# Performance work log

Hardware: AMD Instinct MI355X
Metric: run time of the kernel (lower is better)

Reference implementation:

```python
import jax, jax.numpy as jnp
import numpy as np
import math

Z_DIM = 128
N_HEAD = 4
C = 32
L = 512


def setup_inputs() -> dict:
    key = jax.random.key(0)
    ks = jax.random.split(key, 16)
    s = lambda fan_in: 1.0 / math.sqrt(fan_in)
    hc = N_HEAD * C
    return {
        "z_": jax.random.normal(ks[0], (L, L, Z_DIM), dtype=jnp.float32),
        "ln_g": jnp.ones((Z_DIM,), jnp.float32),
        "ln_b": jnp.zeros((Z_DIM,), jnp.float32),
        "qw": jax.random.normal(ks[1], (Z_DIM, hc), jnp.float32) * s(Z_DIM),
        "qb": jnp.zeros((hc,), jnp.float32),
        "kw": jax.random.normal(ks[2], (Z_DIM, hc), jnp.float32) * s(Z_DIM),
        "kb": jnp.zeros((hc,), jnp.float32),
        "vw": jax.random.normal(ks[3], (Z_DIM, hc), jnp.float32) * s(Z_DIM),
        "vb": jnp.zeros((hc,), jnp.float32),
        "bw": jax.random.normal(ks[4], (Z_DIM, N_HEAD), jnp.float32) * s(Z_DIM),
        "bb": jnp.zeros((N_HEAD,), jnp.float32),
        "gw": jax.random.normal(ks[5], (Z_DIM, hc), jnp.float32) * s(Z_DIM),
        "gb": jnp.zeros((hc,), jnp.float32),
        "ow": jax.random.normal(ks[6], (hc, Z_DIM), jnp.float32) * s(hc),
        "ob": jnp.zeros((Z_DIM,), jnp.float32),
    }


def _layernorm(x, g, b, eps=1e-5):
    mu = jnp.mean(x, axis=-1, keepdims=True)
    var = jnp.var(x, axis=-1, keepdims=True)
    return (x - mu) * jax.lax.rsqrt(var + eps) * g + b


def reference(z_, ln_g, ln_b, qw, qb, kw, kb, vw, vb, bw, bb, gw, gb, ow, ob):
    L1, L2, D = z_.shape
    z = _layernorm(z_, ln_g, ln_b)
    q = (z @ qw + qb).reshape(L1, L2, N_HEAD, C)
    k = (z @ kw + kb).reshape(L1, L2, N_HEAD, C)
    v = (z @ vw + vb).reshape(L1, L2, N_HEAD, C)
    bias = z @ bw + bb  # [L1, L2, H]
    scale = (1.0 / math.sqrt(C)) / math.sqrt(L2)
    # Note: reduction over the leading (row) axis b, per the source einsum.
    att = jnp.einsum('blhc,bkhc->lkh', q, k) * scale + bias  # [L, L, H]
    att = jax.nn.softmax(att, axis=1)
    o = jnp.einsum('lkh,bkhc->blhc', att, v)  # [L1, L2, H, C]
    g = jax.nn.sigmoid((z @ gw + gb).reshape(L1, L2, N_HEAD, C))
    o = (g * o).reshape(L1, L2, N_HEAD * C)
    return o @ ow + ob
```

## Files before the change

### kernel.cpp

```cpp
#include <hip/hip_runtime.h>
#include <hip/hip_bf16.h>
#include <math.h>


#define LL 512
#define ZD 128
#define NROWS (LL*LL)
#define ATT_SCALE (1.0f/128.0f)
#define NSPLIT 8

typedef __attribute__((ext_vector_type(4))) float f32x4;
typedef __attribute__((ext_vector_type(8))) short short8;
typedef __attribute__((ext_vector_type(8))) unsigned short u16x8;

__device__ __forceinline__ unsigned short f2bf(float f){
  union { float f; unsigned u; } v; v.f = f;
  unsigned r = (v.u + 0x7FFFu + ((v.u >> 16) & 1u)) >> 16;
  return (unsigned short)r;
}
__device__ __forceinline__ float bf2f(unsigned short h){
  union { float f; unsigned u; } v; v.u = ((unsigned)h) << 16;
  return v.f;
}

__global__ void k_prep(const float* __restrict__ qw, const float* __restrict__ kw,
                       const float* __restrict__ vw, const float* __restrict__ gw,
                       const float* __restrict__ bw,
                       const float* __restrict__ qb, const float* __restrict__ kb,
                       const float* __restrict__ vb, const float* __restrict__ gb,
                       const float* __restrict__ bb,
                       const float* __restrict__ ow,
                       unsigned short* __restrict__ Wt, unsigned short* __restrict__ Ot,
                       float* __restrict__ biasv){
  int n = blockIdx.x;
  int k = threadIdx.x;
  if (n < 516){
    float v;
    if (n < 128)      v = qw[k*128 + n];
    else if (n < 256) v = kw[k*128 + (n-128)];
    else if (n < 384) v = vw[k*128 + (n-256)];
    else if (n < 512) v = gw[k*128 + (n-384)];
    else              v = bw[k*4   + (n-512)];
    Wt[n*ZD + k] = f2bf(v);
    if (k == 0){
      float bvv;
      if (n < 128)      bvv = qb[n];
      else if (n < 256) bvv = kb[n-128];
      else if (n < 384) bvv = vb[n-256];
      else if (n < 512) bvv = gb[n-384];
      else              bvv = bb[n-512];
      biasv[n] = bvv;
    }
  } else {
    int d = n - 516;
    Ot[d*ZD + k] = f2bf(ow[k*ZD + d]);
  }
}

__launch_bounds__(256, 3)
__global__ void k_proj(const float* __restrict__ z,
                       const float* __restrict__ ln_g, const float* __restrict__ ln_b,
                       const unsigned short* __restrict__ Wt,
                       const float* __restrict__ biasv,
                       unsigned short* __restrict__ qbuf,
                       unsigned short* __restrict__ kbuf,
                       unsigned short* __restrict__ vt,
                       unsigned short* __restrict__ gbuf,
                       float* __restrict__ biasz){
  const int P = 136;
  __shared__ unsigned short As[128*136];
  __shared__ float lng[128], lnb[128];
  __shared__ float lbias[640];
  int t = threadIdx.x;
  long mbase = (long)blockIdx.x * 128;
  int bb_ = (int)(mbase >> 9);
  int rr0 = (int)(mbase & 511);
  if (t < 128){ lng[t] = ln_g[t]; lnb[t] = ln_b[t]; }
  if (t < 160) *(float4*)&lbias[t*4] = *(const float4*)&biasv[t*4];
  {
    int row = t >> 1, half = t & 1;
    const float4* zr = (const float4*)(z + (mbase + row)*ZD + half*64);
    float4 zv[16];
    float s1 = 0.f, s2 = 0.f;
#pragma unroll
    for (int i = 0; i < 16; i++){
      zv[i] = zr[i];
      s1 += zv[i].x + zv[i].y + zv[i].z + zv[i].w;
      s2 += zv[i].x*zv[i].x + zv[i].y*zv[i].y + zv[i].z*zv[i].z + zv[i].w*zv[i].w;
    }
    s1 += __shfl_xor(s1, 1);
    s2 += __shfl_xor(s2, 1);
    float mu = s1 * (1.f/128.f);
    float rs = rsqrtf(s2*(1.f/128.f) - mu*mu + 1e-5f);
    __syncthreads();
#pragma unroll
    for (int i = 0; i < 16; i++){
      int c0 = half*64 + i*4;
      ushort4 pk;
      pk.x = f2bf((zv[i].x - mu)*rs*lng[c0+0] + lnb[c0+0]);
      pk.y = f2bf((zv[i].y - mu)*rs*lng[c0+1] + lnb[c0+1]);
      pk.z = f2bf((zv[i].z - mu)*rs*lng[c0+2] + lnb[c0+2]);
      pk.w = f2bf((zv[i].w - mu)*rs*lng[c0+3] + lnb[c0+3]);
      *(ushort4*)&As[row*P + c0] = pk;
    }
  }
  __syncthreads();
  int w = t >> 6, tl = t & 63;
  int m0 = (w & 1)*64, n0 = (w >> 1)*64;
  int lr = tl & 15, quad = tl >> 4;
#pragma unroll
  for (int nt = 0; nt < 5; nt++){
    f32x4 acc[4][4];
    for (int i=0;i<4;i++) for (int j=0;j<4;j++) acc[i][j] = f32x4{0.f,0.f,0.f,0.f};
    for (int kk = 0; kk < 4; kk++){
      short8 a[4], bq[4];
      for (int i=0;i<4;i++) a[i] = *(const short8*)&As[(m0 + i*16 + lr)*P + kk*32 + quad*8];
      const unsigned short* wp = Wt + ((long)nt*128 + n0 + lr)*ZD + kk*32 + quad*8;
      for (int j=0;j<4;j++) bq[j] = *(const short8*)(wp + (long)j*16*ZD);
      for (int i=0;i<4;i++) for (int j=0;j<4;j++){
        if (nt == 2) acc[i][j] = __builtin_amdgcn_mfma_f32_16x16x32_bf16(a[i], bq[j], acc[i][j], 0,0,0);
        else         acc[i][j] = __builtin_amdgcn_mfma_f32_16x16x32_bf16(bq[j], a[i], acc[i][j], 0,0,0);
      }
    }
    if (nt == 0 || nt == 1 || nt == 3){
      unsigned short* dst = (nt == 0) ? qbuf : (nt == 1) ? kbuf : gbuf;
      float4 bd[4];
#pragma unroll
      for (int j=0;j<4;j++) bd[j] = *(const float4*)&lbias[nt*128 + n0 + j*16 + quad*4];
#pragma unroll
      for (int i=0;i<4;i++){
        long grow = mbase + m0 + i*16 + lr;
#pragma unroll
        for (int j=0;j<4;j++){
          int nc0 = n0 + j*16 + quad*4;
          ushort4 pk;
          pk.x = f2bf(acc[i][j][0] + bd[j].x);
          pk.y = f2bf(acc[i][j][1] + bd[j].y);
          pk.z = f2bf(acc[i][j][2] + bd[j].z);
          pk.w = f2bf(acc[i][j][3] + bd[j].w);
          *(ushort4*)&dst[grow*128 + nc0] = pk;
        }
      }
    } else if (nt == 2){
#pragma unroll
      for (int j=0;j<4;j++){
        int ncol = n0 + j*16 + lr;
        float bv = lbias[256 + ncol];
#pragma unroll
        for (int i=0;i<4;i++){
          int rr = rr0 + m0 + i*16 + quad*4;
          ushort4 pk;
          pk.x = f2bf(acc[i][j][0] + bv);
          pk.y = f2bf(acc[i][j][1] + bv);
          pk.z = f2bf(acc[i][j][2] + bv);
          pk.w = f2bf(acc[i][j][3] + bv);
          *(ushort4*)&vt[((long)bb_*128 + ncol)*512 + rr] = pk;
        }
      }
    } else if (n0 == 0 && quad == 0){
      float4 bd = *(const float4*)&lbias[512];
#pragma unroll
      for (int i=0;i<4;i++){
        long grow = mbase + m0 + i*16 + lr;
        float4 o;
        o.x = acc[i][0][0] + bd.x;
        o.y = acc[i][0][1] + bd.y;
        o.z = acc[i][0][2] + bd.z;
        o.w = acc[i][0][3] + bd.w;
        *(float4*)&biasz[grow*4] = o;
      }
    }
  }
}

__launch_bounds__(256, 3)
__global__ void k_att(const unsigned short* __restrict__ qbuf,
                      const unsigned short* __restrict__ kbuf,
                      float* __restrict__ partial){
  int t = threadIdx.x;
  int ktb = blockIdx.x * 128, ltb = blockIdx.y * 128;
  int split = blockIdx.z >> 2, h = blockIdx.z & 3;
  int w = t >> 6, tl = t & 63;
  int m0 = (w & 1)*64, n0 = (w >> 1)*64;
  int lr = tl & 15, quad = tl >> 4;
  f32x4 acc[4][4];
  for (int i=0;i<4;i++) for (int j=0;j<4;j++) acc[i][j] = f32x4{0.f,0.f,0.f,0.f};
  for (int it = 0; it < 64; it++){
    int b = split*64 + it;
    long qb0 = ((long)b*LL + ltb + m0 + lr)*128 + h*32 + quad*8;
    long kb0 = ((long)b*LL + ktb + n0 + lr)*128 + h*32 + quad*8;
    short8 a[4], bq[4];
#pragma unroll
    for (int i=0;i<4;i++) a[i]  = *(const short8*)&qbuf[qb0 + (long)i*16*128];
#pragma unroll
    for (int i=0;i<4;i++) bq[i] = *(const short8*)&kbuf[kb0 + (long)i*16*128];
#pragma unroll
    for (int i=0;i<4;i++) for (int j=0;j<4;j++)
      acc[i][j] = __builtin_amdgcn_mfma_f32_16x16x32_bf16(a[i], bq[j], acc[i][j], 0,0,0);
  }
  long obase = (((long)(split*4 + h)*LL) + ltb)*512 + ktb;
  for (int i=0;i<4;i++) for (int j=0;j<4;j++){
    int ncol = n0 + j*16 + lr;
    for (int r=0;r<4;r++){
      int mrow = m0 + i*16 + quad*4 + r;
      partial[obase + (long)mrow*512 + ncol] = acc[i][j][r];
    }
  }
}

__global__ void k_soft(const float* __restrict__ partial,
                       const float* __restrict__ biasz,
                       unsigned short* __restrict__ attb){
  int bx = blockIdx.x;
  int h = bx >> 9, l = bx & 511;
  int t = threadIdx.x;
  int k1 = t, k2 = t + 256;
  float v1 = 0.f, v2 = 0.f;
  for (int s = 0; s < NSPLIT; s++){
    long base = (((long)(s*4 + h)*LL) + l)*512;
    v1 += partial[base + k1];
    v2 += partial[base + k2];
  }
  v1 = v1*ATT_SCALE + biasz[((long)l*512 + k1)*4 + h];
  v2 = v2*ATT_SCALE + biasz[((long)l*512 + k2)*4 + h];
  __shared__ float red[4];
  int w = t >> 6, tl = t & 63;
  float mx = fmaxf(v1, v2);
  for (int o = 32; o > 0; o >>= 1) mx = fmaxf(mx, __shfl_xor(mx, o));
  if (tl == 0) red[w] = mx;
  __syncthreads();
  mx = fmaxf(fmaxf(red[0], red[1]), fmaxf(red[2], red[3]));
  __syncthreads();
  float e1 = __expf(v1 - mx), e2 = __expf(v2 - mx);
  float sm = e1 + e2;
  for (int o = 32; o > 0; o >>= 1) sm += __shfl_xor(sm, o);
  if (tl == 0) red[w] = sm;
  __syncthreads();
  sm = red[0] + red[1] + red[2] + red[3];
  float inv = 1.f / sm;
  long ob = ((long)h*LL + l)*512;
  attb[ob + k1] = f2bf(e1*inv);
  attb[ob + k2] = f2bf(e2*inv);
}

__launch_bounds__(256, 3)
__global__ void k_o(const unsigned short* __restrict__ attb,
                    const unsigned short* __restrict__ vt,
                    const unsigned short* __restrict__ gbuf,
                    unsigned short* __restrict__ xbuf){
  int t = threadIdx.x;
  int ltb = blockIdx.x * 128;
  int b   = blockIdx.y;
  int w = t >> 6, tl = t & 63;
  int lr = tl & 15, quad = tl >> 4;
  f32x4 acc[8][2];
  for (int i=0;i<8;i++) for (int j=0;j<2;j++) acc[i][j] = f32x4{0.f,0.f,0.f,0.f};
  long abase0 = ((long)w*LL + ltb + lr)*512;
  long vbase0 = ((long)b*128 + w*32 + lr)*512;
  for (int it = 0; it < 16; it++){
    int kb = it*32 + quad*8;
    short8 a[8], bq[2];
#pragma unroll
    for (int i=0;i<8;i++) a[i]  = *(const short8*)&attb[abase0 + (long)i*16*512 + kb];
#pragma unroll
    for (int j=0;j<2;j++) bq[j] = *(const short8*)&vt[vbase0 + (long)j*16*512 + kb];
#pragma unroll
    for (int i=0;i<8;i++) for (int j=0;j<2;j++)
      acc[i][j] = __builtin_amdgcn_mfma_f32_16x16x32_bf16(a[i], bq[j], acc[i][j], 0,0,0);
  }
  for (int i=0;i<8;i++) for (int j=0;j<2;j++) for (int r=0;r<4;r++){
    int l = i*16 + quad*4 + r;
    int c = j*16 + lr;
    long grow = (long)b*LL + ltb + l;
    float gv = bf2f(gbuf[grow*128 + w*32 + c]);
    float sg = 1.f / (1.f + __expf(-gv));
    xbuf[grow*128 + w*32 + c] = f2bf(acc[i][j][r] * sg);
  }
}

__launch_bounds__(256, 2)
__global__ void k_fin(const unsigned short* __restrict__ xbuf,
                      const unsigned short* __restrict__ Ot,
                      const float* __restrict__ ob,
                      float* __restrict__ out){
  const int P = 136;
  __shared__ unsigned short As[128*136];
  __shared__ unsigned short Bs[128*136];
  int t = threadIdx.x;
  long mbase = (long)blockIdx.x * 128;
  {
    int row = t >> 1, half = t & 1;
    const u16x8* src = (const u16x8*)(xbuf + (mbase + row)*128 + half*64);
    u16x8* dst = (u16x8*)&As[row*P + half*64];
    for (int i=0;i<8;i++) dst[i] = src[i];
    const u16x8* wsrc = (const u16x8*)(Ot + row*128 + half*64);
    u16x8* wdst = (u16x8*)&Bs[row*P + half*64];
    for (int i=0;i<8;i++) wdst[i] = wsrc[i];
  }
  __syncthreads();
  int w = t >> 6, tl = t & 63;
  int m0 = (w & 1)*64, n0 = (w >> 1)*64;
  int lr = tl & 15, quad = tl >> 4;
  f32x4 acc[4][4];
  for (int i=0;i<4;i++) for (int j=0;j<4;j++) acc[i][j] = f32x4{0.f,0.f,0.f,0.f};
  for (int kk = 0; kk < 4; kk++){
    short8 a[4], bq[4];
    for (int i=0;i<4;i++) a[i]  = *(const short8*)&As[(m0 + i*16 + lr)*P + kk*32 + quad*8];
    for (int i=0;i<4;i++) bq[i] = *(const short8*)&Bs[(n0 + i*16 + lr)*P + kk*32 + quad*8];
    for (int i=0;i<4;i++) for (int j=0;j<4;j++)
      acc[i][j] = __builtin_amdgcn_mfma_f32_16x16x32_bf16(a[i], bq[j], acc[i][j], 0,0,0);
  }
  for (int i=0;i<4;i++) for (int j=0;j<4;j++){
    int ncol = n0 + j*16 + lr;
    float bv = ob[ncol];
    for (int r=0;r<4;r++){
      int mrow = m0 + i*16 + quad*4 + r;
      out[(mbase + mrow)*128 + ncol] = acc[i][j][r] + bv;
    }
  }
}

extern "C" void kernel_launch(void* const* d_in, const int* in_sizes, int n_in,
                              void* d_out, int out_size, void* d_ws, size_t ws_size,
                              hipStream_t stream){
  (void)in_sizes; (void)n_in; (void)out_size; (void)ws_size;
  const float* z    = (const float*)d_in[0];
  const float* ln_g = (const float*)d_in[1];
  const float* ln_b = (const float*)d_in[2];
  const float* qw   = (const float*)d_in[3];
  const float* qb   = (const float*)d_in[4];
  const float* kw   = (const float*)d_in[5];
  const float* kb   = (const float*)d_in[6];
  const float* vw   = (const float*)d_in[7];
  const float* vb   = (const float*)d_in[8];
  const float* bw   = (const float*)d_in[9];
  const float* bb   = (const float*)d_in[10];
  const float* gw   = (const float*)d_in[11];
  const float* gb   = (const float*)d_in[12];
  const float* ow   = (const float*)d_in[13];
  const float* ob   = (const float*)d_in[14];
  float* out = (float*)d_out;

  char* wsp = (char*)d_ws;
  unsigned short* Wt    = (unsigned short*)(wsp);
  unsigned short* Ot    = (unsigned short*)(wsp + 163840);
  float*          biasv = (float*)(wsp + 196608);
  unsigned short* qbuf  = (unsigned short*)(wsp + 262144);
  unsigned short* kbuf  = (unsigned short*)(wsp + 262144 + 67108864L);
  unsigned short* vt    = (unsigned short*)(wsp + 262144 + 2*67108864L);
  unsigned short* gbuf  = (unsigned short*)(wsp + 262144 + 3*67108864L);
  char* xreg = wsp + 262144 + 4*67108864L;
  float*          partial = (float*)xreg;
  float*          biasz   = (float*)(xreg + 33554432L);
  unsigned short* xbuf    = (unsigned short*)xreg;
  unsigned short* attb    = (unsigned short*)(xreg + 67108864L);

  k_prep<<<644, 128, 0, stream>>>(qw,kw,vw,gw,bw,qb,kb,vb,gb,bb,ow,Wt,Ot,biasv);
  k_proj<<<2048, 256, 0, stream>>>(z, ln_g, ln_b, Wt, biasv, qbuf, kbuf, vt, gbuf, biasz);
  k_att<<<dim3(4,4,32), 256, 0, stream>>>(qbuf, kbuf, partial);
  k_soft<<<2048, 256, 0, stream>>>(partial, biasz, attb);
  k_o<<<dim3(4,512), 256, 0, stream>>>(attb, vt, gbuf, xbuf);
  k_fin<<<2048, 256, 0, stream>>>(xbuf, Ot, ob, out);
}
```

Measured before the change: 735.3 us.

## Fuse attention-value/gating kernel with output projection via shared memory

```diff
diff --git a/kernel.cpp b/kernel.cpp
--- a/kernel.cpp
+++ b/kernel.cpp
@@ -244,78 +244,82 @@
 }
 
 __launch_bounds__(256, 3)
-__global__ void k_o(const unsigned short* __restrict__ attb,
-                    const unsigned short* __restrict__ vt,
-                    const unsigned short* __restrict__ gbuf,
-                    unsigned short* __restrict__ xbuf){
+__global__ void k_ofin(const unsigned short* __restrict__ attb,
+                       const unsigned short* __restrict__ vt,
+                       const unsigned short* __restrict__ gbuf,
+                       const unsigned short* __restrict__ Ot,
+                       const float* __restrict__ ob,
+                       float* __restrict__ out){
+  const int P = 136;
+  __shared__ unsigned short xs[128*136];
   int t = threadIdx.x;
   int ltb = blockIdx.x * 128;
   int b   = blockIdx.y;
   int w = t >> 6, tl = t & 63;
   int lr = tl & 15, quad = tl >> 4;
-  f32x4 acc[8][2];
-  for (int i=0;i<8;i++) for (int j=0;j<2;j++) acc[i][j] = f32x4{0.f,0.f,0.f,0.f};
-  long abase0 = ((long)w*LL + ltb + lr)*512;
-  long vbase0 = ((long)b*128 + w*32 + lr)*512;
-  for (int it = 0; it < 16; it++){
-    int kb = it*32 + quad*8;
-    short8 a[8], bq[2];
-#pragma unroll
-    for (int i=0;i<8;i++) a[i]  = *(const short8*)&attb[abase0 + (long)i*16*512 + kb];
-#pragma unroll
-    for (int j=0;j<2;j++) bq[j] = *(const short8*)&vt[vbase0 + (long)j*16*512 + kb];
-#pragma unroll
-    for (int i=0;i<8;i++) for (int j=0;j<2;j++)
-      acc[i][j] = __builtin_amdgcn_mfma_f32_16x16x32_bf16(a[i], bq[j], acc[i][j], 0,0,0);
-  }
-  for (int i=0;i<8;i++) for (int j=0;j<2;j++) for (int r=0;r<4;r++){
-    int l = i*16 + quad*4 + r;
-    int c = j*16 + lr;
-    long grow = (long)b*LL + ltb + l;
-    float gv = bf2f(gbuf[grow*128 + w*32 + c]);
-    float sg = 1.f / (1.f + __expf(-gv));
-    xbuf[grow*128 + w*32 + c] = f2bf(acc[i][j][r] * sg);
-  }
-}
-
-__launch_bounds__(256, 2)
-__global__ void k_fin(const unsigned short* __restrict__ xbuf,
-                      const unsigned short* __restrict__ Ot,
-                      const float* __restrict__ ob,
-                      float* __restrict__ out){
-  const int P = 136;
-  __shared__ unsigned short As[128*136];
-  __shared__ unsigned short Bs[128*136];
-  int t = threadIdx.x;
-  long mbase = (long)blockIdx.x * 128;
   {
-    int row = t >> 1, half = t & 1;
-    const u16x8* src = (const u16x8*)(xbuf + (mbase + row)*128 + half*64);
-    u16x8* dst = (u16x8*)&As[row*P + half*64];
-    for (int i=0;i<8;i++) dst[i] = src[i];
-    const u16x8* wsrc = (const u16x8*)(Ot + row*128 + half*64);
-    u16x8* wdst = (u16x8*)&Bs[row*P + half*64];
-    for (int i=0;i<8;i++) wdst[i] = wsrc[i];
-  }
-  __syncthreads();
-  int w = t >> 6, tl = t & 63;
-  int m0 = (w & 1)*64, n0 = (w >> 1)*64;
-  int lr = tl & 15, quad = tl >> 4;
-  f32x4 acc[4][4];
-  for (int i=0;i<4;i++) for (int j=0;j<4;j++) acc[i][j] = f32x4{0.f,0.f,0.f,0.f};
-  for (int kk = 0; kk < 4; kk++){
-    short8 a[4], bq[4];
-    for (int i=0;i<4;i++) a[i]  = *(const short8*)&As[(m0 + i*16 + lr)*P + kk*32 + quad*8];
-    for (int i=0;i<4;i++) bq[i] = *(const short8*)&Bs[(n0 + i*16 + lr)*P + kk*32 + quad*8];
-    for (int i=0;i<4;i++) for (int j=0;j<4;j++)
-      acc[i][j] = __builtin_amdgcn_mfma_f32_16x16x32_bf16(a[i], bq[j], acc[i][j], 0,0,0);
-  }
-  for (int i=0;i<4;i++) for (int j=0;j<4;j++){
-    int ncol = n0 + j*16 + lr;
-    float bv = ob[ncol];
-    for (int r=0;r<4;r++){
-      int mrow = m0 + i*16 + quad*4 + r;
-      out[(mbase + mrow)*128 + ncol] = acc[i][j][r] + bv;
+    f32x4 acc[8][2];
+    for (int i=0;i<8;i++) for (int j=0;j<2;j++) acc[i][j] = f32x4{0.f,0.f,0.f,0.f};
+    long abase0 = ((long)w*LL + ltb + lr)*512;
+    long vbase0 = ((long)b*128 + w*32 + lr)*512;
+    for (int it = 0; it < 16; it++){
+      int kb = it*32 + quad*8;
+      short8 a[8], bq[2];
+#pragma unroll
+      for (int i=0;i<8;i++) a[i]  = *(const short8*)&attb[abase0 + (long)i*16*512 + kb];
+#pragma unroll
+      for (int j=0;j<2;j++) bq[j] = *(const short8*)&vt[vbase0 + (long)j*16*512 + kb];
+#pragma unroll
+      for (int i=0;i<8;i++) for (int j=0;j<2;j++)
+        acc[i][j] = __builtin_amdgcn_mfma_f32_16x16x32_bf16(bq[j], a[i], acc[i][j], 0,0,0);
+    }
+#pragma unroll
+    for (int i=0;i<8;i++){
+      int l = i*16 + lr;
+      long grow = (long)b*LL + ltb + l;
+#pragma unroll
+      for (int j=0;j<2;j++){
+        int c0 = j*16 + quad*4;
+        ushort4 gv = *(const ushort4*)&gbuf[grow*128 + w*32 + c0];
+        ushort4 pk;
+        float g0 = bf2f(gv.x), g1 = bf2f(gv.y), g2 = bf2f(gv.z), g3 = bf2f(gv.w);
+        pk.x = f2bf(acc[i][j][0] / (1.f + __expf(-g0)));
+        pk.y = f2bf(acc[i][j][1] / (1.f + __expf(-g1)));
+        pk.z = f2bf(acc[i][j][2] / (1.f + __expf(-g2)));
+        pk.w = f2bf(acc[i][j][3] / (1.f + __expf(-g3)));
+        *(ushort4*)&xs[l*P + w*32 + c0] = pk;
+      }
+    }
+  }
+  __syncthreads();
+  {
+    int m0 = (w & 1)*64, n0 = (w >> 1)*64;
+    f32x4 acc2[4][4];
+    for (int i=0;i<4;i++) for (int j=0;j<4;j++) acc2[i][j] = f32x4{0.f,0.f,0.f,0.f};
+    for (int kk = 0; kk < 4; kk++){
+      short8 a2[4], b2[4];
+#pragma unroll
+      for (int i=0;i<4;i++) a2[i] = *(const short8*)&xs[(m0 + i*16 + lr)*P + kk*32 + quad*8];
+#pragma unroll
+      for (int j=0;j<4;j++) b2[j] = *(const short8*)&Ot[(n0 + j*16 + lr)*ZD + kk*32 + quad*8];
+#pragma unroll
+      for (int i=0;i<4;i++) for (int j=0;j<4;j++)
+        acc2[i][j] = __builtin_amdgcn_mfma_f32_16x16x32_bf16(b2[j], a2[i], acc2[i][j], 0,0,0);
+    }
+#pragma unroll
+    for (int i=0;i<4;i++){
+      long grow = (long)b*LL + ltb + m0 + i*16 + lr;
+#pragma unroll
+      for (int j=0;j<4;j++){
+        int d0 = n0 + j*16 + quad*4;
+        float4 bv = *(const float4*)&ob[d0];
+        float4 o;
+        o.x = acc2[i][j][0] + bv.x;
+        o.y = acc2[i][j][1] + bv.y;
+        o.z = acc2[i][j][2] + bv.z;
+        o.w = acc2[i][j][3] + bv.w;
+        *(float4*)&out[grow*128 + d0] = o;
+      }
     }
   }
 }
@@ -352,13 +356,11 @@
   char* xreg = wsp + 262144 + 4*67108864L;
   float*          partial = (float*)xreg;
   float*          biasz   = (float*)(xreg + 33554432L);
-  unsigned short* xbuf    = (unsigned short*)xreg;
   unsigned short* attb    = (unsigned short*)(xreg + 67108864L);
 
   k_prep<<<644, 128, 0, stream>>>(qw,kw,vw,gw,bw,qb,kb,vb,gb,bb,ow,Wt,Ot,biasv);
   k_proj<<<2048, 256, 0, stream>>>(z, ln_g, ln_b, Wt, biasv, qbuf, kbuf, vt, gbuf, biasz);
   k_att<<<dim3(4,4,32), 256, 0, stream>>>(qbuf, kbuf, partial);
   k_soft<<<2048, 256, 0, stream>>>(partial, biasz, attb);
-  k_o<<<dim3(4,512), 256, 0, stream>>>(attb, vt, gbuf, xbuf);
-  k_fin<<<2048, 256, 0, stream>>>(xbuf, Ot, ob, out);
-}
+  k_ofin<<<dim3(4,512), 256, 0, stream>>>(attb, vt, gbuf, Ot, ob, out);
+}
```

Measured after the change: 708.9 us. 3.6% less time.
